# Kernel tuning notes

Measured on AMD Instinct MI355X. Metric: run time of the kernel, lower is better.

Reference implementation:

```python
import jax, jax.numpy as jnp
import numpy as np

H = 64; W = 64; P = 16; NPH = 4; NPW = 4; PH = 16; PW = 16; ZD = 32; HD = 1024; UD = 3; B = 256


def affine_grid(theta, Ho, Wo):
    # torch F.affine_grid, align_corners=False. theta [N,2,3] -> grid [N,Ho,Wo,2]
    xs = (2.0 * jnp.arange(Wo, dtype=theta.dtype) + 1.0) / Wo - 1.0
    ys = (2.0 * jnp.arange(Ho, dtype=theta.dtype) + 1.0) / Ho - 1.0
    X, Y = jnp.meshgrid(xs, ys)  # [Ho,Wo] each, x varies along last axis
    base = jnp.stack([X, Y, jnp.ones_like(X)], axis=-1)  # [Ho,Wo,3]
    return jnp.einsum('nij,hwj->nhwi', theta, base)


def grid_sample(img, grid):
    # torch F.grid_sample bilinear, padding_mode='zeros', align_corners=False
    # img [N,H,W], grid [N,Ho,Wo,2] in [-1,1]
    Hi, Wi = img.shape[1], img.shape[2]
    x = (grid[..., 0] + 1.0) * Wi / 2.0 - 0.5
    y = (grid[..., 1] + 1.0) * Hi / 2.0 - 0.5
    x0 = jnp.floor(x); y0 = jnp.floor(y)
    wx = x - x0; wy = y - y0

    def gather(ix, iy):
        valid = (ix >= 0) & (ix < Wi) & (iy >= 0) & (iy < Hi)
        ixc = jnp.clip(ix, 0, Wi - 1).astype(jnp.int32)
        iyc = jnp.clip(iy, 0, Hi - 1).astype(jnp.int32)
        v = jax.vmap(lambda im, yy, xx: im[yy, xx])(img, iyc, ixc)
        return jnp.where(valid, v, 0.0)

    return (gather(x0, y0) * (1 - wx) * (1 - wy)
            + gather(x0 + 1, y0) * wx * (1 - wy)
            + gather(x0, y0 + 1) * (1 - wx) * wy
            + gather(x0 + 1, y0 + 1) * wx * wy)


def rot_tr(u):
    # rotTrMatrix: u [N,3] (angle, tx, ty) -> [N,2,3]
    c = jnp.cos(u[:, 0]); s = jnp.sin(u[:, 0])
    R = jnp.stack([jnp.stack([c, -s], -1), jnp.stack([s, c], -1)], -2)  # [N,2,2]
    return jnp.concatenate([R, u[:, 1:3, None]], axis=2)


def anchor_theta():
    # anchor_move: identity rotation + per-part grid-cell-center translations
    tx = (np.arange(NPW) * (W / NPW) + W / NPW / 2) / W - 0.5
    ty = (np.arange(NPH) * (H / NPH) + H / NPH / 2) / H - 0.5
    th = np.tile(np.concatenate([np.eye(2), np.zeros((2, 1))], axis=1)[None], (P, 1, 1)).astype(np.float32)
    for k in range(P):
        th[k, 0, 2] = tx[k % NPW]
        th[k, 1, 2] = ty[k // NPW]
    return jnp.asarray(th)


def forward(inputs, W1, b1, W2, b2, Wum, bum, Wuv, buv, Wgm, bgm, Wgv, bgv, Wz, M, eps_u, eps_g):
    hid = jax.nn.relu(inputs.reshape(-1, H * W) @ W1 + b1)
    hid = jax.nn.relu(hid @ W2 + b2)
    # global transform distribution (note: F.threshold(x,-6,6) -> 6 where x<=-6)
    gmu = jnp.tanh(hid @ Wgm + bgm)
    gpre = hid @ Wgv + bgv
    gvar = jnp.exp(jnp.where(gpre > -6.0, gpre, 6.0))
    gu = gmu + gvar * eps_g  # sample_u uses mu + var*eps (var, not std) as in source
    # per-part transform distribution (F.threshold(x,-6,-6) -> clamp below at -6)
    umu = jnp.tanh(hid @ Wum + bum)
    upre = hid @ Wuv + buv
    uvar = jnp.exp(jnp.where(upre > -6.0, upre, -6.0))
    u = (umu + uvar * eps_u).reshape(-1, UD)  # [B*P,3]
    # decode parts (input is ones, as in source)
    parts = jax.nn.sigmoid(jnp.ones((B, ZD), inputs.dtype) @ Wz).reshape(B * P, PH, PW)
    padh = (H - PH) // 2; padw = (W - PW) // 2
    parts = jnp.pad(parts, ((0, 0), (padh, H - PH - padh), (padw, W - PW - padw)))
    # anchor placement of parts and kernel masks
    th_a = jnp.tile(anchor_theta(), (B, 1, 1))  # [B*P,2,3], part-minor ordering
    g_a = affine_grid(th_a, H, W)
    parts = grid_sample(parts, g_a)                     # [B*P,H,W]
    KM = grid_sample(M[:B * P].reshape(B * P, H, W), g_a)
    # per-part rotation+translation for parts; translation-only for kernel
    theta = rot_tr(u)                                   # [B*P,2,3]
    g = affine_grid(theta, H, W)
    eye = jnp.broadcast_to(jnp.eye(2, dtype=theta.dtype), (B * P, 2, 2))
    theta_K = jnp.concatenate([eye, theta[:, :, 2:3]], axis=2)
    g_K = affine_grid(theta_K, H, W)
    KM = grid_sample(KM, g_K).reshape(B, P, H, W)
    xp = grid_sample(parts, g).reshape(B, P, H, W)
    # masked weighted compositing
    num = jnp.sum(xp * KM, axis=1)
    den = jnp.sum(KM, axis=1)
    den = jnp.where(den == 0.0, 1.0, den)
    x = num / den
    # global transform
    theta_g = rot_tr(gu)
    g_g = affine_grid(theta_g, H, W)
    return grid_sample(x, g_g)[:, None]  # [B,1,H,W]


def setup_inputs() -> dict:
    key = jax.random.key(0)
    ks = jax.random.split(key, 18)

    def lin(k, fin, fout):
        return jax.random.normal(k, (fin, fout), jnp.float32) / np.sqrt(fin)

    return {
        'inputs': jax.random.uniform(ks[0], (B, H * W), jnp.float32),
        'W1': lin(ks[1], H * W, HD), 'b1': jnp.zeros((HD,), jnp.float32),
        'W2': lin(ks[2], HD, HD), 'b2': jnp.zeros((HD,), jnp.float32),
        'Wum': lin(ks[3], HD, P * UD), 'bum': jnp.zeros((P * UD,), jnp.float32),
        'Wuv': lin(ks[4], HD, P * UD), 'buv': jnp.zeros((P * UD,), jnp.float32),
        'Wgm': lin(ks[5], HD, UD), 'bgm': jnp.zeros((UD,), jnp.float32),
        'Wgv': lin(ks[6], HD, UD), 'bgv': jnp.zeros((UD,), jnp.float32),
        'Wz': lin(ks[7], ZD, P * PH * PW),
        'M': jax.random.uniform(ks[8], (B * P, 1, H, W), jnp.float32),
        'eps_u': jax.random.normal(ks[9], (B, P * UD), jnp.float32),
        'eps_g': jax.random.normal(ks[10], (B, UD), jnp.float32),
    }


def reference(inputs, W1, b1, W2, b2, Wum, bum, Wuv, buv, Wgm, bgm, Wgv, bgv, Wz, M, eps_u, eps_g):
    return forward(inputs, W1, b1, W2, b2, Wum, bum, Wuv, buv, Wgm, bgm, Wgv, bgv, Wz, M, eps_u, eps_g)
```

## Files before the change

kernel.cpp:

```cpp
#include <hip/hip_runtime.h>
#include <math.h>

#define SPLITK 8
#define PSUM_STRIDE 262144

typedef __bf16 bf16x8 __attribute__((ext_vector_type(8)));
typedef float  f32x16 __attribute__((ext_vector_type(16)));

__device__ __forceinline__ unsigned short bf16rne(float x) {
    unsigned int u = __float_as_uint(x);
    unsigned int r = u + 0x7FFFu + ((u >> 16) & 1u);
    return (unsigned short)(r >> 16);
}
__device__ __forceinline__ float bf16tof(unsigned short h) {
    return __uint_as_float(((unsigned int)h) << 16);
}

__global__ __launch_bounds__(256) void prep_all(
    const float* __restrict__ inputs,
    const float* __restrict__ W1, const float* __restrict__ W2,
    const float* __restrict__ Wum, const float* __restrict__ Wuv,
    const float* __restrict__ Wgm, const float* __restrict__ Wgv,
    const float* __restrict__ Wz,
    unsigned short* __restrict__ Ahi, unsigned short* __restrict__ Alo,
    unsigned short* __restrict__ W1Thi, unsigned short* __restrict__ W1Tlo,
    unsigned short* __restrict__ W2Thi, unsigned short* __restrict__ W2Tlo,
    float* __restrict__ WT, float* __restrict__ partsb)
{
    __shared__ float t[32][33];
    int bid = blockIdx.x;
    int tid = threadIdx.x;
    if (bid < 4096 || (bid >= 5120 && bid < 6144)) {
        const float* W = (bid < 4096) ? W1 : W2;
        unsigned short* Thi = (bid < 4096) ? W1Thi : W2Thi;
        unsigned short* Tlo = (bid < 4096) ? W1Tlo : W2Tlo;
        int K = (bid < 4096) ? 4096 : 1024;
        int b2 = (bid < 4096) ? bid : (bid - 5120);
        int n0 = (b2 & 31) * 32, k0 = (b2 >> 5) * 32;
        int c = tid & 31, r0 = tid >> 5;
#pragma unroll
        for (int i = 0; i < 4; i++)
            t[r0 + 8 * i][c] = W[(size_t)(k0 + r0 + 8 * i) * 1024 + n0 + c];
        __syncthreads();
        int kk = tid & 31, n1 = tid >> 5;
#pragma unroll
        for (int i = 0; i < 4; i++) {
            float x = t[kk][n1 + 8 * i];
            unsigned short h = bf16rne(x);
            unsigned short l = bf16rne(x - bf16tof(h));
            size_t o = (size_t)(n0 + n1 + 8 * i) * K + k0 + kk;
            Thi[o] = h;
            Tlo[o] = l;
        }
    } else if (bid < 5120) {
        int id = ((bid - 4096) * 256 + tid) * 4;
        float4 x = *(const float4*)(inputs + id);
        ushort4 h, l;
        h.x = bf16rne(x.x); l.x = bf16rne(x.x - bf16tof(h.x));
        h.y = bf16rne(x.y); l.y = bf16rne(x.y - bf16tof(h.y));
        h.z = bf16rne(x.z); l.z = bf16rne(x.z - bf16tof(h.z));
        h.w = bf16rne(x.w); l.w = bf16rne(x.w - bf16tof(h.w));
        *(ushort4*)(Ahi + id) = h;
        *(ushort4*)(Alo + id) = l;
    } else if (bid < 6552) {
        int id = (bid - 6144) * 256 + tid;
        int o = id >> 10;
        int k = id & 1023;
        float v;
        if (o < 48)       v = Wum[k * 48 + o];
        else if (o < 96)  v = Wuv[k * 48 + (o - 48)];
        else if (o < 99)  v = Wgm[k * 3 + (o - 96)];
        else              v = Wgv[k * 3 + (o - 99)];
        WT[id] = v;
    } else {
        int idx = (bid - 6552) * 256 + tid;
        float s = 0.f;
#pragma unroll
        for (int z = 0; z < 32; z++) s += Wz[z * 4096 + idx];
        partsb[idx] = 1.f / (1.f + expf(-s));
    }
}

__global__ __launch_bounds__(256) void gemm_bf16x3(
    const unsigned short* __restrict__ Ahi, const unsigned short* __restrict__ Alo,
    const unsigned short* __restrict__ Bhi, const unsigned short* __restrict__ Blo,
    float* __restrict__ psum, int K, int kchunk)
{
    __shared__ unsigned short Ah[4096], Al[4096], Bh[4096], Bl[4096];
    int tid = threadIdx.x;
    int n0 = blockIdx.x * 64, m0 = blockIdx.y * 64;
    int kb = blockIdx.z * kchunk;
    int wid = tid >> 6, lane = tid & 63;
    int wm = wid & 1, wn = wid >> 1;
    int lr = lane & 31, hi = lane >> 5;

    int r0 = tid >> 3, ch0 = tid & 7;
    int r1 = (tid + 256) >> 3, ch1 = (tid + 256) & 7;
    int l0 = r0 * 64 + 8 * (ch0 ^ (r0 & 7));
    int l1 = r1 * 64 + 8 * (ch1 ^ (r1 & 7));
    size_t ga0 = (size_t)(m0 + r0) * K + kb + ch0 * 8;
    size_t ga1 = (size_t)(m0 + r1) * K + kb + ch1 * 8;
    size_t gb0 = (size_t)(n0 + r0) * K + kb + ch0 * 8;
    size_t gb1 = (size_t)(n0 + r1) * K + kb + ch1 * 8;

    f32x16 acc_hh = {}, acc_hl = {}, acc_lh = {};

    int nkt = kchunk >> 6;
    uint4 vah0, vah1, val0, val1, vbh0, vbh1, vbl0, vbl1;
    vah0 = *(const uint4*)(Ahi + ga0);
    vah1 = *(const uint4*)(Ahi + ga1);
    val0 = *(const uint4*)(Alo + ga0);
    val1 = *(const uint4*)(Alo + ga1);
    vbh0 = *(const uint4*)(Bhi + gb0);
    vbh1 = *(const uint4*)(Bhi + gb1);
    vbl0 = *(const uint4*)(Blo + gb0);
    vbl1 = *(const uint4*)(Blo + gb1);

    int basea = (wm * 32 + lr) * 64;
    int baseb = (wn * 32 + lr) * 64;
    int sw = lr & 7;

    for (int kt = 0; kt < nkt; kt++) {
        __syncthreads();
        *(uint4*)(Ah + l0) = vah0;
        *(uint4*)(Ah + l1) = vah1;
        *(uint4*)(Al + l0) = val0;
        *(uint4*)(Al + l1) = val1;
        *(uint4*)(Bh + l0) = vbh0;
        *(uint4*)(Bh + l1) = vbh1;
        *(uint4*)(Bl + l0) = vbl0;
        *(uint4*)(Bl + l1) = vbl1;
        __syncthreads();
        if (kt + 1 < nkt) {
            size_t o = (size_t)(kt + 1) * 64;
            vah0 = *(const uint4*)(Ahi + ga0 + o);
            vah1 = *(const uint4*)(Ahi + ga1 + o);
            val0 = *(const uint4*)(Alo + ga0 + o);
            val1 = *(const uint4*)(Alo + ga1 + o);
            vbh0 = *(const uint4*)(Bhi + gb0 + o);
            vbh1 = *(const uint4*)(Bhi + gb1 + o);
            vbl0 = *(const uint4*)(Blo + gb0 + o);
            vbl1 = *(const uint4*)(Blo + gb1 + o);
        }
#pragma unroll
        for (int s = 0; s < 4; s++) {
            int cidx = 8 * (((s << 1) + hi) ^ sw);
            bf16x8 afh = *(const bf16x8*)(Ah + basea + cidx);
            bf16x8 afl = *(const bf16x8*)(Al + basea + cidx);
            bf16x8 bfh = *(const bf16x8*)(Bh + baseb + cidx);
            bf16x8 bfl = *(const bf16x8*)(Bl + baseb + cidx);
            acc_hh = __builtin_amdgcn_mfma_f32_32x32x16_bf16(afh, bfh, acc_hh, 0, 0, 0);
            acc_hl = __builtin_amdgcn_mfma_f32_32x32x16_bf16(afh, bfl, acc_hl, 0, 0, 0);
            acc_lh = __builtin_amdgcn_mfma_f32_32x32x16_bf16(afl, bfh, acc_lh, 0, 0, 0);
        }
    }

    float* op = psum + (size_t)blockIdx.z * PSUM_STRIDE;
    int colg = n0 + wn * 32 + lr;
#pragma unroll
    for (int r = 0; r < 16; r++) {
        int rowl = (r & 3) + 8 * (r >> 2) + 4 * hi;
        op[(size_t)(m0 + wm * 32 + rowl) * 1024 + colg] = acc_hh[r] + acc_hl[r] + acc_lh[r];
    }
}

__global__ __launch_bounds__(256) void reduce_bias_relu_split(
    const float* __restrict__ psum, const float* __restrict__ bias,
    unsigned short* __restrict__ hi, unsigned short* __restrict__ lo)
{
    int i = (blockIdx.x * 256 + threadIdx.x) * 4;
    float4 v = *(const float4*)(psum + i);
#pragma unroll
    for (int s = 1; s < SPLITK; s++) {
        float4 t = *(const float4*)(psum + (size_t)s * PSUM_STRIDE + i);
        v.x += t.x; v.y += t.y; v.z += t.z; v.w += t.w;
    }
    float4 bb = *(const float4*)(bias + (i & 1023));
    v.x = fmaxf(v.x + bb.x, 0.f);
    v.y = fmaxf(v.y + bb.y, 0.f);
    v.z = fmaxf(v.z + bb.z, 0.f);
    v.w = fmaxf(v.w + bb.w, 0.f);
    ushort4 h, l;
    h.x = bf16rne(v.x); l.x = bf16rne(v.x - bf16tof(h.x));
    h.y = bf16rne(v.y); l.y = bf16rne(v.y - bf16tof(h.y));
    h.z = bf16rne(v.z); l.z = bf16rne(v.z - bf16tof(h.z));
    h.w = bf16rne(v.w); l.w = bf16rne(v.w - bf16tof(h.w));
    *(ushort4*)(hi + i) = h;
    *(ushort4*)(lo + i) = l;
}

__global__ __launch_bounds__(1024) void composite_heads(
    const float* __restrict__ psum, const float* __restrict__ b2,
    const float* __restrict__ WT,
    const float* __restrict__ bum, const float* __restrict__ buv,
    const float* __restrict__ bgm, const float* __restrict__ bgv,
    const float* __restrict__ eps_u, const float* __restrict__ eps_g,
    const float* __restrict__ M, const float* __restrict__ parts,
    float* __restrict__ out)
{
    __shared__ float patch[4096];
    __shared__ float plane[2][4096];
    __shared__ float h2[1024];
    __shared__ float u_raw[51];
    __shared__ float pc[16], psn[16], ptx[16], pty[16], pwx[16], pwy[16];
    __shared__ int pix[16], piy[16];
    int b = blockIdx.x;
    int tid = threadIdx.x;

    {
        float v = psum[(size_t)b * 1024 + tid];
#pragma unroll
        for (int s = 1; s < SPLITK; s++)
            v += psum[(size_t)s * PSUM_STRIDE + (size_t)b * 1024 + tid];
        h2[tid] = fmaxf(v + b2[tid], 0.f);
    }
    for (int i = tid; i < 4096; i += 1024) patch[i] = parts[i];
    __syncthreads();

    {
        int w = tid >> 6, l = tid & 63;
        const float4* h4 = (const float4*)h2;
        float4 hr0 = h4[l], hr1 = h4[64 + l], hr2 = h4[128 + l], hr3 = h4[192 + l];
        for (int o = w; o < 51; o += 16) {
            int rm = (o < 48) ? o : (48 + o);
            int rv = (o < 48) ? (o + 48) : (51 + o);
            const float* wpm = WT + rm * 1024 + l * 4;
            const float* wpv = WT + rv * 1024 + l * 4;
            float4 wm0 = *(const float4*)(wpm);
            float4 wm1 = *(const float4*)(wpm + 256);
            float4 wm2 = *(const float4*)(wpm + 512);
            float4 wm3 = *(const float4*)(wpm + 768);
            float4 wv0 = *(const float4*)(wpv);
            float4 wv1 = *(const float4*)(wpv + 256);
            float4 wv2 = *(const float4*)(wpv + 512);
            float4 wv3 = *(const float4*)(wpv + 768);
            float am = 0.f, av = 0.f;
            am = fmaf(hr0.x, wm0.x, am); am = fmaf(hr0.y, wm0.y, am);
            am = fmaf(hr0.z, wm0.z, am); am = fmaf(hr0.w, wm0.w, am);
            av = fmaf(hr0.x, wv0.x, av); av = fmaf(hr0.y, wv0.y, av);
            av = fmaf(hr0.z, wv0.z, av); av = fmaf(hr0.w, wv0.w, av);
            am = fmaf(hr1.x, wm1.x, am); am = fmaf(hr1.y, wm1.y, am);
            am = fmaf(hr1.z, wm1.z, am); am = fmaf(hr1.w, wm1.w, am);
            av = fmaf(hr1.x, wv1.x, av); av = fmaf(hr1.y, wv1.y, av);
            av = fmaf(hr1.z, wv1.z, av); av = fmaf(hr1.w, wv1.w, av);
            am = fmaf(hr2.x, wm2.x, am); am = fmaf(hr2.y, wm2.y, am);
            am = fmaf(hr2.z, wm2.z, am); am = fmaf(hr2.w, wm2.w, am);
            av = fmaf(hr2.x, wv2.x, av); av = fmaf(hr2.y, wv2.y, av);
            av = fmaf(hr2.z, wv2.z, av); av = fmaf(hr2.w, wv2.w, av);
            am = fmaf(hr3.x, wm3.x, am); am = fmaf(hr3.y, wm3.y, am);
            am = fmaf(hr3.z, wm3.z, am); am = fmaf(hr3.w, wm3.w, am);
            av = fmaf(hr3.x, wv3.x, av); av = fmaf(hr3.y, wv3.y, av);
            av = fmaf(hr3.w, wv3.w, av); av = fmaf(hr3.z, wv3.z, av);
#pragma unroll
            for (int s = 32; s; s >>= 1) {
                am += __shfl_xor(am, s, 64);
                av += __shfl_xor(av, s, 64);
            }
            if (l == 0) {
                if (o < 48) {
                    float umu = tanhf(am + bum[o]);
                    float uvar = expf(fmaxf(av + buv[o], -6.f));
                    u_raw[o] = umu + uvar * eps_u[b * 48 + o];
                } else {
                    int n = o - 48;
                    float gmu = tanhf(am + bgm[n]);
                    float gpre = av + bgv[n];
                    float gvar = expf(gpre > -6.f ? gpre : 6.f);
                    u_raw[o] = gmu + gvar * eps_g[b * 3 + n];
                }
            }
        }
    }
    __syncthreads();

    if (tid < 16) {
        float ang = u_raw[tid * 3 + 0];
        float tx = u_raw[tid * 3 + 1], ty = u_raw[tid * 3 + 2];
        pc[tid] = cosf(ang);
        psn[tid] = sinf(ang);
        ptx[tid] = tx;
        pty[tid] = ty;
        float ax = fminf(fmaxf(32.f * tx, -16384.f), 16384.f);
        float fax = floorf(ax);
        pwx[tid] = ax - fax;
        pix[tid] = (int)fax;
        float ay = fminf(fmaxf(32.f * ty, -16384.f), 16384.f);
        float fay = floorf(ay);
        pwy[tid] = ay - fay;
        piy[tid] = (int)fay;
    }
    const float* Mb = M + ((size_t)(b * 16) << 12);
    ((float4*)plane[0])[tid] = ((const float4*)Mb)[tid];
    float4 pfn = ((const float4*)(Mb + 4096))[tid];
    __syncthreads();

    int j = tid & 63;
    int i0 = (tid >> 6) * 4;
    float xnv = (float)(2 * j + 1) * (1.f / 64.f) - 1.f;
    float ynv0 = (float)(2 * i0 + 1) * (1.f / 64.f) - 1.f;

    float num[4] = {}, den[4] = {};
    float* pl_cur = plane[0];
    float* pl_nxt = plane[1];

    for (int p = 0; p < 16; p++) {
        if (p + 1 < 16) ((float4*)pl_nxt)[tid] = pfn;
        if (p + 2 < 16) pfn = ((const float4*)(Mb + ((size_t)(p + 2) << 12)))[tid];

        int dx = 8 * (p & 3) - 12;
        int dy = 8 * (p >> 2) - 12;
        float c = pc[p], s = psn[p], tx = ptx[p], ty = pty[p];
        float wx = pwx[p], wy = pwy[p];
        int ix = pix[p], iy = piy[p];
        int iY = iy + dy;

        int x0 = j + ix;
        int X = x0 + dx;
        bool vc0 = ((unsigned)x0 < 64u) && ((unsigned)X < 64u);
        bool vc1 = ((unsigned)(x0 + 1) < 64u) && ((unsigned)(X + 1) < 64u);
        float w0 = vc0 ? (1.f - wx) : 0.f;
        float w1 = vc1 ? wx : 0.f;
        int Xc0 = min(max(X, 0), 63);
        int Xc1 = min(max(X + 1, 0), 63);

        const float* pl = pl_cur;
        float R[5];
#pragma unroll
        for (int r = 0; r < 5; r++) {
            int i = i0 + r;
            int ri = i + iY;
            bool vr = ((unsigned)(i + iy) < 64u) && ((unsigned)ri < 64u);
            int ric = min(max(ri, 0), 63);
            const float* row = pl + (ric << 6);
            float val = fmaf(w0, row[Xc0], w1 * row[Xc1]);
            R[r] = vr ? val : 0.f;
        }

        float gx0 = fmaf(-s, ynv0, fmaf(c, xnv, tx));
        float gy0 = fmaf(c, ynv0, fmaf(s, xnv, ty));
        float xs = fmaf(gx0, 32.f, 31.5f);
        float ysv = fmaf(gy0, 32.f, 31.5f);
        int ox = 24 - dx, oy = 24 - dy;
        float oxf = (float)ox, oyf = (float)oy;
        const float* pp = patch + (p << 8);
#pragma unroll
        for (int r = 0; r < 4; r++) {
            float km = fmaf(wy, R[r + 1] - R[r], R[r]);
            den[r] += km;

            if (xs >= oxf - 1.f && xs < oxf + 16.f &&
                ysv >= oyf - 1.f && ysv < oyf + 16.f) {
                float xf = floorf(xs), yf = floorf(ysv);
                float wxx = xs - xf, wyy = ysv - yf;
                int a0 = (int)yf - oy;
                int b0c = (int)xf - ox;
                float v00 = 0.f, v10 = 0.f, v01 = 0.f, v11 = 0.f;
                if ((unsigned)a0 < 16u) {
                    const float* pr = pp + a0 * 16;
                    if ((unsigned)b0c < 16u) v00 = pr[b0c];
                    if ((unsigned)(b0c + 1) < 16u) v10 = pr[b0c + 1];
                }
                if ((unsigned)(a0 + 1) < 16u) {
                    const float* pr = pp + (a0 + 1) * 16;
                    if ((unsigned)b0c < 16u) v01 = pr[b0c];
                    if ((unsigned)(b0c + 1) < 16u) v11 = pr[b0c + 1];
                }
                float top = fmaf(wxx, v10 - v00, v00);
                float bot = fmaf(wxx, v11 - v01, v01);
                float xp = fmaf(wyy, bot - top, top);
                num[r] = fmaf(xp, km, num[r]);
            }
            xs -= s;
            ysv += c;
        }
        __syncthreads();
        float* tmp = pl_cur; pl_cur = pl_nxt; pl_nxt = tmp;
    }

    float* xl = plane[0];
#pragma unroll
    for (int r = 0; r < 4; r++) {
        float d = (den[r] == 0.f) ? 1.f : den[r];
        xl[(i0 + r) * 64 + j] = num[r] / d;
    }
    __syncthreads();

    float ang = u_raw[48], gtx = u_raw[49], gty = u_raw[50];
    float cg = cosf(ang), sg = sinf(ang);
    float* ob = out + ((size_t)b << 12);
#pragma unroll
    for (int r = 0; r < 4; r++) {
        int i = i0 + r;
        float ynv = (float)(2 * i + 1) * (1.f / 64.f) - 1.f;
        float gx = cg * xnv - sg * ynv + gtx;
        float gy = sg * xnv + cg * ynv + gty;
        gx = fminf(fmaxf(gx, -8.f), 8.f);
        gy = fminf(fmaxf(gy, -8.f), 8.f);
        float xs = fmaf(gx, 32.f, 31.5f);
        float ysv = fmaf(gy, 32.f, 31.5f);
        float xf = floorf(xs), yf = floorf(ysv);
        float wx = xs - xf, wy = ysv - yf;
        int x0 = (int)xf, y0 = (int)yf;
        float v00 = 0.f, v10 = 0.f, v01 = 0.f, v11 = 0.f;
        bool vx0 = (unsigned)x0 < 64u, vx1 = (unsigned)(x0 + 1) < 64u;
        if ((unsigned)y0 < 64u) {
            const float* row = xl + y0 * 64;
            if (vx0) v00 = row[x0];
            if (vx1) v10 = row[x0 + 1];
        }
        if ((unsigned)(y0 + 1) < 64u) {
            const float* row = xl + (y0 + 1) * 64;
            if (vx0) v01 = row[x0];
            if (vx1) v11 = row[x0 + 1];
        }
        float top = fmaf(wx, v10 - v00, v00);
        float bot = fmaf(wx, v11 - v01, v01);
        ob[i * 64 + j] = fmaf(wy, bot - top, top);
    }
}

extern "C" void kernel_launch(void* const* d_in, const int* in_sizes, int n_in,
                              void* d_out, int out_size, void* d_ws, size_t ws_size,
                              hipStream_t stream)
{
    (void)in_sizes; (void)n_in; (void)out_size; (void)ws_size;
    const float* inputs = (const float*)d_in[0];
    const float* W1  = (const float*)d_in[1];
    const float* b1  = (const float*)d_in[2];
    const float* W2  = (const float*)d_in[3];
    const float* b2  = (const float*)d_in[4];
    const float* Wum = (const float*)d_in[5];
    const float* bum = (const float*)d_in[6];
    const float* Wuv = (const float*)d_in[7];
    const float* buv = (const float*)d_in[8];
    const float* Wgm = (const float*)d_in[9];
    const float* bgm = (const float*)d_in[10];
    const float* Wgv = (const float*)d_in[11];
    const float* bgv = (const float*)d_in[12];
    const float* Wz  = (const float*)d_in[13];
    const float* Mm  = (const float*)d_in[14];
    const float* eps_u = (const float*)d_in[15];
    const float* eps_g = (const float*)d_in[16];

    float* ws = (float*)d_ws;
    float* psum      = ws;
    float* parts_buf = psum + 8 * PSUM_STRIDE;
    float* WTh_buf   = parts_buf + 4096;
    unsigned short* us = (unsigned short*)(WTh_buf + 104448);
    unsigned short* Ahi   = us;
    unsigned short* Alo   = Ahi + 1048576;
    unsigned short* W1Thi = Alo + 1048576;
    unsigned short* W1Tlo = W1Thi + 4194304;
    unsigned short* W2Thi = W1Tlo + 4194304;
    unsigned short* W2Tlo = W2Thi + 1048576;
    unsigned short* H1hi  = W2Tlo + 1048576;
    unsigned short* H1lo  = H1hi + 262144;

    prep_all<<<6568, 256, 0, stream>>>(inputs, W1, W2, Wum, Wuv, Wgm, Wgv, Wz,
                                       Ahi, Alo, W1Thi, W1Tlo, W2Thi, W2Tlo,
                                       WTh_buf, parts_buf);

    gemm_bf16x3<<<dim3(16, 4, SPLITK), 256, 0, stream>>>(Ahi, Alo, W1Thi, W1Tlo,
                                                         psum, 4096, 4096 / SPLITK);
    reduce_bias_relu_split<<<256, 256, 0, stream>>>(psum, b1, H1hi, H1lo);
    gemm_bf16x3<<<dim3(16, 4, SPLITK), 256, 0, stream>>>(H1hi, H1lo, W2Thi, W2Tlo,
                                                         psum, 1024, 1024 / SPLITK);
    composite_heads<<<256, 1024, 0, stream>>>(psum, b2, WTh_buf, bum, buv,
                                              bgm, bgv, eps_u, eps_g,
                                              Mm, parts_buf, (float*)d_out);
}
```

Measured before the change: 193.8 us.

## Batch mask-plane loads into two 8-plane LDS phases with early prefetch

The composite kernel now stages the 16 mask planes in two groups of eight instead of double-buffering one plane at a time. The first eight are loaded into registers at kernel start, so their latency overlaps the head computation, and the second eight are prefetched while the first group is composited. This cuts the per-part __syncthreads from 16 to a few barriers. It raises LDS use to about 150KB per block and register pressure (8 float4 staging registers), which can limit occupancy.

Result: slower. 222.9 us (+15.1%).

```diff
diff --git a/kernel.cpp b/kernel.cpp
--- a/kernel.cpp
+++ b/kernel.cpp
@@ -199,13 +199,20 @@
     float* __restrict__ out)
 {
     __shared__ float patch[4096];
-    __shared__ float plane[2][4096];
+    __shared__ float planes[8][4096];
     __shared__ float h2[1024];
     __shared__ float u_raw[51];
     __shared__ float pc[16], psn[16], ptx[16], pty[16], pwx[16], pwy[16];
     __shared__ int pix[16], piy[16];
     int b = blockIdx.x;
     int tid = threadIdx.x;
+
+    const float* Mb = M + ((size_t)(b * 16) << 12);
+
+    float4 st[8];
+#pragma unroll
+    for (int q = 0; q < 8; q++)
+        st[q] = ((const float4*)(Mb + (size_t)q * 4096))[tid];
 
     {
         float v = psum[(size_t)b * 1024 + tid];
@@ -250,7 +257,7 @@
             am = fmaf(hr3.x, wm3.x, am); am = fmaf(hr3.y, wm3.y, am);
             am = fmaf(hr3.z, wm3.z, am); am = fmaf(hr3.w, wm3.w, am);
             av = fmaf(hr3.x, wv3.x, av); av = fmaf(hr3.y, wv3.y, av);
-            av = fmaf(hr3.w, wv3.w, av); av = fmaf(hr3.z, wv3.z, av);
+            av = fmaf(hr3.z, wv3.z, av); av = fmaf(hr3.w, wv3.w, av);
 #pragma unroll
             for (int s = 32; s; s >>= 1) {
                 am += __shfl_xor(am, s, 64);
@@ -289,9 +296,12 @@
         pwy[tid] = ay - fay;
         piy[tid] = (int)fay;
     }
-    const float* Mb = M + ((size_t)(b * 16) << 12);
-    ((float4*)plane[0])[tid] = ((const float4*)Mb)[tid];
-    float4 pfn = ((const float4*)(Mb + 4096))[tid];
+
+#pragma unroll
+    for (int q = 0; q < 8; q++) ((float4*)planes[q])[tid] = st[q];
+#pragma unroll
+    for (int q = 0; q < 8; q++)
+        st[q] = ((const float4*)(Mb + (size_t)(8 + q) * 4096))[tid];
     __syncthreads();
 
     int j = tid & 63;
@@ -300,84 +310,86 @@
     float ynv0 = (float)(2 * i0 + 1) * (1.f / 64.f) - 1.f;
 
     float num[4] = {}, den[4] = {};
-    float* pl_cur = plane[0];
-    float* pl_nxt = plane[1];
-
-    for (int p = 0; p < 16; p++) {
-        if (p + 1 < 16) ((float4*)pl_nxt)[tid] = pfn;
-        if (p + 2 < 16) pfn = ((const float4*)(Mb + ((size_t)(p + 2) << 12)))[tid];
-
-        int dx = 8 * (p & 3) - 12;
-        int dy = 8 * (p >> 2) - 12;
-        float c = pc[p], s = psn[p], tx = ptx[p], ty = pty[p];
-        float wx = pwx[p], wy = pwy[p];
-        int ix = pix[p], iy = piy[p];
-        int iY = iy + dy;
-
-        int x0 = j + ix;
-        int X = x0 + dx;
-        bool vc0 = ((unsigned)x0 < 64u) && ((unsigned)X < 64u);
-        bool vc1 = ((unsigned)(x0 + 1) < 64u) && ((unsigned)(X + 1) < 64u);
-        float w0 = vc0 ? (1.f - wx) : 0.f;
-        float w1 = vc1 ? wx : 0.f;
-        int Xc0 = min(max(X, 0), 63);
-        int Xc1 = min(max(X + 1, 0), 63);
-
-        const float* pl = pl_cur;
-        float R[5];
-#pragma unroll
-        for (int r = 0; r < 5; r++) {
-            int i = i0 + r;
-            int ri = i + iY;
-            bool vr = ((unsigned)(i + iy) < 64u) && ((unsigned)ri < 64u);
-            int ric = min(max(ri, 0), 63);
-            const float* row = pl + (ric << 6);
-            float val = fmaf(w0, row[Xc0], w1 * row[Xc1]);
-            R[r] = vr ? val : 0.f;
-        }
-
-        float gx0 = fmaf(-s, ynv0, fmaf(c, xnv, tx));
-        float gy0 = fmaf(c, ynv0, fmaf(s, xnv, ty));
-        float xs = fmaf(gx0, 32.f, 31.5f);
-        float ysv = fmaf(gy0, 32.f, 31.5f);
-        int ox = 24 - dx, oy = 24 - dy;
-        float oxf = (float)ox, oyf = (float)oy;
-        const float* pp = patch + (p << 8);
-#pragma unroll
-        for (int r = 0; r < 4; r++) {
-            float km = fmaf(wy, R[r + 1] - R[r], R[r]);
-            den[r] += km;
-
-            if (xs >= oxf - 1.f && xs < oxf + 16.f &&
-                ysv >= oyf - 1.f && ysv < oyf + 16.f) {
-                float xf = floorf(xs), yf = floorf(ysv);
-                float wxx = xs - xf, wyy = ysv - yf;
-                int a0 = (int)yf - oy;
-                int b0c = (int)xf - ox;
-                float v00 = 0.f, v10 = 0.f, v01 = 0.f, v11 = 0.f;
-                if ((unsigned)a0 < 16u) {
-                    const float* pr = pp + a0 * 16;
-                    if ((unsigned)b0c < 16u) v00 = pr[b0c];
-                    if ((unsigned)(b0c + 1) < 16u) v10 = pr[b0c + 1];
-                }
-                if ((unsigned)(a0 + 1) < 16u) {
-                    const float* pr = pp + (a0 + 1) * 16;
-                    if ((unsigned)b0c < 16u) v01 = pr[b0c];
-                    if ((unsigned)(b0c + 1) < 16u) v11 = pr[b0c + 1];
-                }
-                float top = fmaf(wxx, v10 - v00, v00);
-                float bot = fmaf(wxx, v11 - v01, v01);
-                float xp = fmaf(wyy, bot - top, top);
-                num[r] = fmaf(xp, km, num[r]);
-            }
-            xs -= s;
-            ysv += c;
-        }
-        __syncthreads();
-        float* tmp = pl_cur; pl_cur = pl_nxt; pl_nxt = tmp;
-    }
-
-    float* xl = plane[0];
+
+#define COMP_PART(p) do {                                                     \
+        int dx = 8 * ((p) & 3) - 12;                                          \
+        int dy = 8 * ((p) >> 2) - 12;                                         \
+        float c = pc[p], s = psn[p], tx = ptx[p], ty = pty[p];                \
+        float wx = pwx[p], wy = pwy[p];                                       \
+        int ix = pix[p], iy = piy[p];                                         \
+        int iY = iy + dy;                                                     \
+        int x0 = j + ix;                                                      \
+        int X = x0 + dx;                                                      \
+        bool vc0 = ((unsigned)x0 < 64u) && ((unsigned)X < 64u);               \
+        bool vc1 = ((unsigned)(x0 + 1) < 64u) && ((unsigned)(X + 1) < 64u);   \
+        float w0 = vc0 ? (1.f - wx) : 0.f;                                    \
+        float w1 = vc1 ? wx : 0.f;                                            \
+        int Xc0 = min(max(X, 0), 63);                                         \
+        int Xc1 = min(max(X + 1, 0), 63);                                     \
+        const float* pl = planes[(p) & 7];                                    \
+        float R[5];                                                           \
+        _Pragma("unroll")                                                     \
+        for (int r = 0; r < 5; r++) {                                         \
+            int i = i0 + r;                                                   \
+            int ri = i + iY;                                                  \
+            bool vr = ((unsigned)(i + iy) < 64u) && ((unsigned)ri < 64u);     \
+            int ric = min(max(ri, 0), 63);                                    \
+            const float* row = pl + (ric << 6);                               \
+            float val = fmaf(w0, row[Xc0], w1 * row[Xc1]);                    \
+            R[r] = vr ? val : 0.f;                                            \
+        }                                                                     \
+        float gx0 = fmaf(-s, ynv0, fmaf(c, xnv, tx));                         \
+        float gy0 = fmaf(c, ynv0, fmaf(s, xnv, ty));                          \
+        float xs = fmaf(gx0, 32.f, 31.5f);                                    \
+        float ysv = fmaf(gy0, 32.f, 31.5f);                                   \
+        int ox = 24 - dx, oy = 24 - dy;                                       \
+        float oxf = (float)ox, oyf = (float)oy;                               \
+        const float* pp = patch + ((p) << 8);                                 \
+        _Pragma("unroll")                                                     \
+        for (int r = 0; r < 4; r++) {                                         \
+            float km = fmaf(wy, R[r + 1] - R[r], R[r]);                       \
+            den[r] += km;                                                     \
+            if (xs >= oxf - 1.f && xs < oxf + 16.f &&                         \
+                ysv >= oyf - 1.f && ysv < oyf + 16.f) {                       \
+                float xf = floorf(xs), yf = floorf(ysv);                      \
+                float wxx = xs - xf, wyy = ysv - yf;                          \
+                int a0 = (int)yf - oy;                                        \
+                int b0c = (int)xf - ox;                                       \
+                float v00 = 0.f, v10 = 0.f, v01 = 0.f, v11 = 0.f;             \
+                if ((unsigned)a0 < 16u) {                                     \
+                    const float* pr = pp + a0 * 16;                           \
+                    if ((unsigned)b0c < 16u) v00 = pr[b0c];                   \
+                    if ((unsigned)(b0c + 1) < 16u) v10 = pr[b0c + 1];         \
+                }                                                             \
+                if ((unsigned)(a0 + 1) < 16u) {                               \
+                    const float* pr = pp + (a0 + 1) * 16;                     \
+                    if ((unsigned)b0c < 16u) v01 = pr[b0c];                   \
+                    if ((unsigned)(b0c + 1) < 16u) v11 = pr[b0c + 1];         \
+                }                                                             \
+                float top = fmaf(wxx, v10 - v00, v00);                        \
+                float bot = fmaf(wxx, v11 - v01, v01);                        \
+                float xp = fmaf(wyy, bot - top, top);                         \
+                num[r] = fmaf(xp, km, num[r]);                                \
+            }                                                                 \
+            xs -= s;                                                          \
+            ysv += c;                                                         \
+        }                                                                     \
+    } while (0)
+
+#pragma unroll
+    for (int p = 0; p < 8; p++) COMP_PART(p);
+
+    __syncthreads();
+#pragma unroll
+    for (int q = 0; q < 8; q++) ((float4*)planes[q])[tid] = st[q];
+    __syncthreads();
+
+#pragma unroll
+    for (int p = 8; p < 16; p++) COMP_PART(p);
+#undef COMP_PART
+
+    __syncthreads();
+    float* xl = planes[0];
 #pragma unroll
     for (int r = 0; r < 4; r++) {
         float d = (den[r] == 0.f) ? 1.f : den[r];
```

## Split composite into two half-image blocks per batch and move W2 prep off critical path

Applied to the files above, without the earlier changes.

The single 256-block composite kernel is split into 512 blocks of 512 threads, each computing half the image rows. The intermediate image and global transform params go to a workspace, and a new final_transform kernel applies the global rotation. W2 transpose, head-weight transpose and part sigmoid move from the first prep kernel into the reduce kernel so the first GEMM can start sooner. In exchange, each half-block recomputes the MLP heads and loads all M planes, and there is an extra launch plus a global round trip.

Result: slower. 204.9 us (+5.8%).

```diff
diff --git a/kernel.cpp b/kernel.cpp
--- a/kernel.cpp
+++ b/kernel.cpp
@@ -16,31 +16,20 @@
     return __uint_as_float(((unsigned int)h) << 16);
 }
 
-__global__ __launch_bounds__(256) void prep_all(
-    const float* __restrict__ inputs,
-    const float* __restrict__ W1, const float* __restrict__ W2,
-    const float* __restrict__ Wum, const float* __restrict__ Wuv,
-    const float* __restrict__ Wgm, const float* __restrict__ Wgv,
-    const float* __restrict__ Wz,
+__global__ __launch_bounds__(256) void prepA(
+    const float* __restrict__ inputs, const float* __restrict__ W1,
     unsigned short* __restrict__ Ahi, unsigned short* __restrict__ Alo,
-    unsigned short* __restrict__ W1Thi, unsigned short* __restrict__ W1Tlo,
-    unsigned short* __restrict__ W2Thi, unsigned short* __restrict__ W2Tlo,
-    float* __restrict__ WT, float* __restrict__ partsb)
+    unsigned short* __restrict__ W1Thi, unsigned short* __restrict__ W1Tlo)
 {
     __shared__ float t[32][33];
     int bid = blockIdx.x;
     int tid = threadIdx.x;
-    if (bid < 4096 || (bid >= 5120 && bid < 6144)) {
-        const float* W = (bid < 4096) ? W1 : W2;
-        unsigned short* Thi = (bid < 4096) ? W1Thi : W2Thi;
-        unsigned short* Tlo = (bid < 4096) ? W1Tlo : W2Tlo;
-        int K = (bid < 4096) ? 4096 : 1024;
-        int b2 = (bid < 4096) ? bid : (bid - 5120);
-        int n0 = (b2 & 31) * 32, k0 = (b2 >> 5) * 32;
+    if (bid < 4096) {
+        int n0 = (bid & 31) * 32, k0 = (bid >> 5) * 32;
         int c = tid & 31, r0 = tid >> 5;
 #pragma unroll
         for (int i = 0; i < 4; i++)
-            t[r0 + 8 * i][c] = W[(size_t)(k0 + r0 + 8 * i) * 1024 + n0 + c];
+            t[r0 + 8 * i][c] = W1[(size_t)(k0 + r0 + 8 * i) * 1024 + n0 + c];
         __syncthreads();
         int kk = tid & 31, n1 = tid >> 5;
 #pragma unroll
@@ -48,11 +37,11 @@
             float x = t[kk][n1 + 8 * i];
             unsigned short h = bf16rne(x);
             unsigned short l = bf16rne(x - bf16tof(h));
-            size_t o = (size_t)(n0 + n1 + 8 * i) * K + k0 + kk;
-            Thi[o] = h;
-            Tlo[o] = l;
-        }
-    } else if (bid < 5120) {
+            size_t o = (size_t)(n0 + n1 + 8 * i) * 4096 + k0 + kk;
+            W1Thi[o] = h;
+            W1Tlo[o] = l;
+        }
+    } else {
         int id = ((bid - 4096) * 256 + tid) * 4;
         float4 x = *(const float4*)(inputs + id);
         ushort4 h, l;
@@ -62,22 +51,6 @@
         h.w = bf16rne(x.w); l.w = bf16rne(x.w - bf16tof(h.w));
         *(ushort4*)(Ahi + id) = h;
         *(ushort4*)(Alo + id) = l;
-    } else if (bid < 6552) {
-        int id = (bid - 6144) * 256 + tid;
-        int o = id >> 10;
-        int k = id & 1023;
-        float v;
-        if (o < 48)       v = Wum[k * 48 + o];
-        else if (o < 96)  v = Wuv[k * 48 + (o - 48)];
-        else if (o < 99)  v = Wgm[k * 3 + (o - 96)];
-        else              v = Wgv[k * 3 + (o - 99)];
-        WT[id] = v;
-    } else {
-        int idx = (bid - 6552) * 256 + tid;
-        float s = 0.f;
-#pragma unroll
-        for (int z = 0; z < 32; z++) s += Wz[z * 4096 + idx];
-        partsb[idx] = 1.f / (1.f + expf(-s));
     }
 }
 
@@ -164,39 +137,84 @@
     }
 }
 
-__global__ __launch_bounds__(256) void reduce_bias_relu_split(
+__global__ __launch_bounds__(256) void reduce_plus(
     const float* __restrict__ psum, const float* __restrict__ bias,
-    unsigned short* __restrict__ hi, unsigned short* __restrict__ lo)
+    unsigned short* __restrict__ hi, unsigned short* __restrict__ lo,
+    const float* __restrict__ W2,
+    unsigned short* __restrict__ W2Thi, unsigned short* __restrict__ W2Tlo,
+    const float* __restrict__ Wum, const float* __restrict__ Wuv,
+    const float* __restrict__ Wgm, const float* __restrict__ Wgv,
+    const float* __restrict__ Wz,
+    float* __restrict__ WT, float* __restrict__ partsb)
 {
-    int i = (blockIdx.x * 256 + threadIdx.x) * 4;
-    float4 v = *(const float4*)(psum + i);
-#pragma unroll
-    for (int s = 1; s < SPLITK; s++) {
-        float4 t = *(const float4*)(psum + (size_t)s * PSUM_STRIDE + i);
-        v.x += t.x; v.y += t.y; v.z += t.z; v.w += t.w;
-    }
-    float4 bb = *(const float4*)(bias + (i & 1023));
-    v.x = fmaxf(v.x + bb.x, 0.f);
-    v.y = fmaxf(v.y + bb.y, 0.f);
-    v.z = fmaxf(v.z + bb.z, 0.f);
-    v.w = fmaxf(v.w + bb.w, 0.f);
-    ushort4 h, l;
-    h.x = bf16rne(v.x); l.x = bf16rne(v.x - bf16tof(h.x));
-    h.y = bf16rne(v.y); l.y = bf16rne(v.y - bf16tof(h.y));
-    h.z = bf16rne(v.z); l.z = bf16rne(v.z - bf16tof(h.z));
-    h.w = bf16rne(v.w); l.w = bf16rne(v.w - bf16tof(h.w));
-    *(ushort4*)(hi + i) = h;
-    *(ushort4*)(lo + i) = l;
-}
-
-__global__ __launch_bounds__(1024) void composite_heads(
+    __shared__ float t[32][33];
+    int bid = blockIdx.x;
+    int tid = threadIdx.x;
+    if (bid < 256) {
+        int i = (bid * 256 + tid) * 4;
+        float4 v = *(const float4*)(psum + i);
+#pragma unroll
+        for (int s = 1; s < SPLITK; s++) {
+            float4 tt = *(const float4*)(psum + (size_t)s * PSUM_STRIDE + i);
+            v.x += tt.x; v.y += tt.y; v.z += tt.z; v.w += tt.w;
+        }
+        float4 bb = *(const float4*)(bias + (i & 1023));
+        v.x = fmaxf(v.x + bb.x, 0.f);
+        v.y = fmaxf(v.y + bb.y, 0.f);
+        v.z = fmaxf(v.z + bb.z, 0.f);
+        v.w = fmaxf(v.w + bb.w, 0.f);
+        ushort4 h, l;
+        h.x = bf16rne(v.x); l.x = bf16rne(v.x - bf16tof(h.x));
+        h.y = bf16rne(v.y); l.y = bf16rne(v.y - bf16tof(h.y));
+        h.z = bf16rne(v.z); l.z = bf16rne(v.z - bf16tof(h.z));
+        h.w = bf16rne(v.w); l.w = bf16rne(v.w - bf16tof(h.w));
+        *(ushort4*)(hi + i) = h;
+        *(ushort4*)(lo + i) = l;
+    } else if (bid < 1280) {
+        int b2 = bid - 256;
+        int n0 = (b2 & 31) * 32, k0 = (b2 >> 5) * 32;
+        int c = tid & 31, r0 = tid >> 5;
+#pragma unroll
+        for (int i = 0; i < 4; i++)
+            t[r0 + 8 * i][c] = W2[(size_t)(k0 + r0 + 8 * i) * 1024 + n0 + c];
+        __syncthreads();
+        int kk = tid & 31, n1 = tid >> 5;
+#pragma unroll
+        for (int i = 0; i < 4; i++) {
+            float x = t[kk][n1 + 8 * i];
+            unsigned short h = bf16rne(x);
+            unsigned short l = bf16rne(x - bf16tof(h));
+            size_t o = (size_t)(n0 + n1 + 8 * i) * 1024 + k0 + kk;
+            W2Thi[o] = h;
+            W2Tlo[o] = l;
+        }
+    } else if (bid < 1688) {
+        int id = (bid - 1280) * 256 + tid;
+        int o = id >> 10;
+        int k = id & 1023;
+        float v;
+        if (o < 48)       v = Wum[k * 48 + o];
+        else if (o < 96)  v = Wuv[k * 48 + (o - 48)];
+        else if (o < 99)  v = Wgm[k * 3 + (o - 96)];
+        else              v = Wgv[k * 3 + (o - 99)];
+        WT[id] = v;
+    } else {
+        int idx = (bid - 1688) * 256 + tid;
+        float s = 0.f;
+#pragma unroll
+        for (int z = 0; z < 32; z++) s += Wz[z * 4096 + idx];
+        partsb[idx] = 1.f / (1.f + expf(-s));
+    }
+}
+
+__global__ __launch_bounds__(512) void composite_half(
     const float* __restrict__ psum, const float* __restrict__ b2,
     const float* __restrict__ WT,
     const float* __restrict__ bum, const float* __restrict__ buv,
     const float* __restrict__ bgm, const float* __restrict__ bgv,
     const float* __restrict__ eps_u, const float* __restrict__ eps_g,
     const float* __restrict__ M, const float* __restrict__ parts,
-    float* __restrict__ out)
+    float* __restrict__ xl_out, float* __restrict__ gu_out)
 {
     __shared__ float patch[4096];
     __shared__ float plane[2][4096];
@@ -204,24 +222,27 @@
     __shared__ float u_raw[51];
     __shared__ float pc[16], psn[16], ptx[16], pty[16], pwx[16], pwy[16];
     __shared__ int pix[16], piy[16];
-    int b = blockIdx.x;
+    int bx = blockIdx.x;
+    int b = bx & 255, hf = bx >> 8;
     int tid = threadIdx.x;
 
-    {
-        float v = psum[(size_t)b * 1024 + tid];
+#pragma unroll
+    for (int e = 0; e < 2; e++) {
+        int idx = tid + e * 512;
+        float v = psum[(size_t)b * 1024 + idx];
 #pragma unroll
         for (int s = 1; s < SPLITK; s++)
-            v += psum[(size_t)s * PSUM_STRIDE + (size_t)b * 1024 + tid];
-        h2[tid] = fmaxf(v + b2[tid], 0.f);
-    }
-    for (int i = tid; i < 4096; i += 1024) patch[i] = parts[i];
+            v += psum[(size_t)s * PSUM_STRIDE + (size_t)b * 1024 + idx];
+        h2[idx] = fmaxf(v + b2[idx], 0.f);
+    }
+    for (int i = tid; i < 4096; i += 512) patch[i] = parts[i];
     __syncthreads();
 
     {
         int w = tid >> 6, l = tid & 63;
         const float4* h4 = (const float4*)h2;
         float4 hr0 = h4[l], hr1 = h4[64 + l], hr2 = h4[128 + l], hr3 = h4[192 + l];
-        for (int o = w; o < 51; o += 16) {
+        for (int o = w; o < 51; o += 8) {
             int rm = (o < 48) ? o : (48 + o);
             int rv = (o < 48) ? (o + 48) : (51 + o);
             const float* wpm = WT + rm * 1024 + l * 4;
@@ -250,7 +271,7 @@
             am = fmaf(hr3.x, wm3.x, am); am = fmaf(hr3.y, wm3.y, am);
             am = fmaf(hr3.z, wm3.z, am); am = fmaf(hr3.w, wm3.w, am);
             av = fmaf(hr3.x, wv3.x, av); av = fmaf(hr3.y, wv3.y, av);
-            av = fmaf(hr3.w, wv3.w, av); av = fmaf(hr3.z, wv3.z, av);
+            av = fmaf(hr3.z, wv3.z, av); av = fmaf(hr3.w, wv3.w, av);
 #pragma unroll
             for (int s = 32; s; s >>= 1) {
                 am += __shfl_xor(am, s, 64);
@@ -266,7 +287,9 @@
                     float gmu = tanhf(am + bgm[n]);
                     float gpre = av + bgv[n];
                     float gvar = expf(gpre > -6.f ? gpre : 6.f);
-                    u_raw[o] = gmu + gvar * eps_g[b * 3 + n];
+                    float gv = gmu + gvar * eps_g[b * 3 + n];
+                    u_raw[o] = gv;
+                    gu_out[b * 3 + n] = gv;
                 }
             }
         }
@@ -291,11 +314,13 @@
     }
     const float* Mb = M + ((size_t)(b * 16) << 12);
     ((float4*)plane[0])[tid] = ((const float4*)Mb)[tid];
-    float4 pfn = ((const float4*)(Mb + 4096))[tid];
+    ((float4*)plane[0])[tid + 512] = ((const float4*)Mb)[tid + 512];
+    float4 pf0 = ((const float4*)(Mb + 4096))[tid];
+    float4 pf1 = ((const float4*)(Mb + 4096))[tid + 512];
     __syncthreads();
 
     int j = tid & 63;
-    int i0 = (tid >> 6) * 4;
+    int i0 = hf * 32 + (tid >> 6) * 4;
     float xnv = (float)(2 * j + 1) * (1.f / 64.f) - 1.f;
     float ynv0 = (float)(2 * i0 + 1) * (1.f / 64.f) - 1.f;
 
@@ -304,8 +329,14 @@
     float* pl_nxt = plane[1];
 
     for (int p = 0; p < 16; p++) {
-        if (p + 1 < 16) ((float4*)pl_nxt)[tid] = pfn;
-        if (p + 2 < 16) pfn = ((const float4*)(Mb + ((size_t)(p + 2) << 12)))[tid];
+        if (p + 1 < 16) {
+            ((float4*)pl_nxt)[tid] = pf0;
+            ((float4*)pl_nxt)[tid + 512] = pf1;
+        }
+        if (p + 2 < 16) {
+            pf0 = ((const float4*)(Mb + ((size_t)(p + 2) << 12)))[tid];
+            pf1 = ((const float4*)(Mb + ((size_t)(p + 2) << 12)))[tid + 512];
+        }
 
         int dx = 8 * (p & 3) - 12;
         int dy = 8 * (p >> 2) - 12;
@@ -377,15 +408,29 @@
         float* tmp = pl_cur; pl_cur = pl_nxt; pl_nxt = tmp;
     }
 
-    float* xl = plane[0];
+    float* xo = xl_out + ((size_t)b << 12);
 #pragma unroll
     for (int r = 0; r < 4; r++) {
         float d = (den[r] == 0.f) ? 1.f : den[r];
-        xl[(i0 + r) * 64 + j] = num[r] / d;
-    }
+        xo[(i0 + r) * 64 + j] = num[r] / d;
+    }
+}
+
+__global__ __launch_bounds__(1024) void final_transform(
+    const float* __restrict__ xl_in, const float* __restrict__ gu,
+    float* __restrict__ out)
+{
+    __shared__ float xl[4096];
+    int b = blockIdx.x;
+    int tid = threadIdx.x;
+    ((float4*)xl)[tid] = ((const float4*)(xl_in + ((size_t)b << 12)))[tid];
     __syncthreads();
 
-    float ang = u_raw[48], gtx = u_raw[49], gty = u_raw[50];
+    int j = tid & 63;
+    int i0 = (tid >> 6) * 4;
+    float xnv = (float)(2 * j + 1) * (1.f / 64.f) - 1.f;
+
+    float ang = gu[b * 3 + 0], gtx = gu[b * 3 + 1], gty = gu[b * 3 + 2];
     float cg = cosf(ang), sg = sinf(ang);
     float* ob = out + ((size_t)b << 12);
 #pragma unroll
@@ -455,17 +500,21 @@
     unsigned short* W2Tlo = W2Thi + 1048576;
     unsigned short* H1hi  = W2Tlo + 1048576;
     unsigned short* H1lo  = H1hi + 262144;
-
-    prep_all<<<6568, 256, 0, stream>>>(inputs, W1, W2, Wum, Wuv, Wgm, Wgv, Wz,
-                                       Ahi, Alo, W1Thi, W1Tlo, W2Thi, W2Tlo,
-                                       WTh_buf, parts_buf);
+    float* xl_buf = (float*)(H1lo + 262144);
+    float* gu_buf = xl_buf + 1048576;
+
+    prepA<<<5120, 256, 0, stream>>>(inputs, W1, Ahi, Alo, W1Thi, W1Tlo);
 
     gemm_bf16x3<<<dim3(16, 4, SPLITK), 256, 0, stream>>>(Ahi, Alo, W1Thi, W1Tlo,
                                                          psum, 4096, 4096 / SPLITK);
-    reduce_bias_relu_split<<<256, 256, 0, stream>>>(psum, b1, H1hi, H1lo);
+    reduce_plus<<<1704, 256, 0, stream>>>(psum, b1, H1hi, H1lo,
+                                          W2, W2Thi, W2Tlo,
+                                          Wum, Wuv, Wgm, Wgv, Wz,
+                                          WTh_buf, parts_buf);
     gemm_bf16x3<<<dim3(16, 4, SPLITK), 256, 0, stream>>>(H1hi, H1lo, W2Thi, W2Tlo,
                                                          psum, 1024, 1024 / SPLITK);
-    composite_heads<<<256, 1024, 0, stream>>>(psum, b2, WTh_buf, bum, buv,
-                                              bgm, bgv, eps_u, eps_g,
-                                              Mm, parts_buf, (float*)d_out);
-}
+    composite_half<<<512, 512, 0, stream>>>(psum, b2, WTh_buf, bum, buv,
+                                            bgm, bgv, eps_u, eps_g,
+                                            Mm, parts_buf, xl_buf, gu_buf);
+    final_transform<<<256, 1024, 0, stream>>>(xl_buf, gu_buf, (float*)d_out);
+}
```
